# Performance work log

Hardware: AMD Instinct MI355X
Metric: run time of the kernel (lower is better)

Reference implementation:

```python
import jax, jax.numpy as jnp
import numpy as np

EOS_IDX = 2
B, LAYERS, HEADS, SEQ = 1, 33, 20, 512


def setup_inputs() -> dict:
    key = jax.random.key(0)
    k1, k2, k3, k4 = jax.random.split(key, 4)
    tokens = jax.random.randint(k1, (B, SEQ), 0, 30)
    attentions = jax.random.normal(k2, (B, LAYERS, HEADS, SEQ, SEQ), dtype=jnp.float32)
    weight = jax.random.normal(k3, (LAYERS * HEADS,), dtype=jnp.float32) * 0.05
    bias = jax.random.normal(k4, (1,), dtype=jnp.float32) * 0.05
    return {"tokens": tokens, "attentions": attentions, "weight": weight, "bias": bias}


def reference(tokens, attentions, weight, bias):
    b, nl, nh, s, _ = attentions.shape
    # mask out positions at/after EOS token pairs
    eos = (tokens != EOS_IDX).astype(attentions.dtype)           # [B, S]
    mask2d = eos[:, None, :] * eos[:, :, None]                   # [B, S, S]
    att = attentions * mask2d[:, None, None, :, :]
    # [..., :-1, :-1] then [..., 1:, 1:] == drop first and last positions
    att = att[..., 1:-1, 1:-1]                                   # [B, L, H, S-2, S-2]
    att = att.reshape(b, nl * nh, s - 2, s - 2)                  # [B, F, s2, s2]
    # symmetrize
    sym = att + jnp.swapaxes(att, -1, -2)
    # average product correction
    a1 = sym.sum(-1, keepdims=True)                              # [B, F, s2, 1]
    a2 = sym.sum(-2, keepdims=True)                              # [B, F, 1, s2]
    a12 = sym.sum((-1, -2), keepdims=True)                       # [B, F, 1, 1]
    norm = sym - a1 * a2 / a12
    logits = jnp.einsum('bfij,f->bij', norm, weight) + bias[0]
    return jax.nn.sigmoid(logits)                                # [B, s2, s2]
```

## Files before the change

kernel.cpp:

```cpp
#include <hip/hip_runtime.h>
#include <math.h>

#define SEQ   512
#define NF    660
#define CROP  510
#define EOSI  2
#define RT    16
#define GH    20
#define NT_   32
#define NG    33

typedef float f4 __attribute__((ext_vector_type(4)));
typedef float f2 __attribute__((ext_vector_type(2)));

#define BARRIER_LGKM() asm volatile("s_waitcnt lgkmcnt(0)\n\ts_barrier" ::: "memory")

#define LOADP(buf, f, prow) do {                                              \
    const float* _b = A + ((size_t)(f) << 18) + ((size_t)(prow) << 9);        \
    buf[0] = *(const f4*)(_b + 4 * lane);                                     \
    buf[1] = *(const f4*)(_b + 256 + 4 * lane);                               \
    buf[2] = *(const f4*)(_b + 512 + 4 * lane);                               \
    buf[3] = *(const f4*)(_b + 768 + 4 * lane);                               \
} while (0)

#define COMP(buf, wf, cacc, wa, POFF, h) do {                                 \
    _Pragma("unroll")                                                         \
    for (int rr = 0; rr < 2; ++rr) {                                          \
        const float mi = mrow[(POFF) * 2 + rr];                               \
        f4 x0 = buf[2 * rr], x1 = buf[2 * rr + 1];                            \
        float vals[8] = {x0[0], x0[1], x0[2], x0[3],                          \
                         x1[0], x1[1], x1[2], x1[3]};                         \
        float rs = 0.f;                                                       \
        _Pragma("unroll")                                                     \
        for (int e = 0; e < 8; ++e) {                                         \
            const float v = vals[e];                                          \
            wa[rr][e] += (wf) * v;                                            \
            rs += mskv[e] * v;                                                \
            cacc[e] += mi * v;                                                \
        }                                                                     \
        _Pragma("unroll")                                                     \
        for (int off = 32; off > 0; off >>= 1)                                \
            rs += __shfl_down(rs, off, 64);                                   \
        if (lane == 0)                                                        \
            rowstage[h][wave * 4 + (POFF) * 2 + rr] = rs;                     \
    }                                                                         \
} while (0)

__global__ __launch_bounds__(256) void pass1_kernel(
    const float* __restrict__ A, const int* __restrict__ tokens,
    const float* __restrict__ weight,
    float* __restrict__ WApart, float* __restrict__ rowsum, float* __restrict__ colpart)
{
    __shared__ float msk[SEQ];
    __shared__ float col_lds[2][4][SEQ];
    __shared__ float colstage[GH][SEQ];
    __shared__ float rowstage[GH][RT];

    const int t = blockIdx.x, g = blockIdx.y;
    const int tid = threadIdx.x, wave = tid >> 6, lane = tid & 63;

    for (int j = tid; j < SEQ; j += 256)
        msk[j] = (j >= 1 && j <= SEQ - 2 && tokens[j] != EOSI) ? 1.f : 0.f;
    BARRIER_LGKM();

    float mskv[8];
    #pragma unroll
    for (int e = 0; e < 8; ++e)
        mskv[e] = msk[(e >> 2) * 256 + 4 * lane + (e & 3)];

    const int row0 = t * RT + wave * 4;
    const float mrow[4] = {msk[row0], msk[row0 + 1], msk[row0 + 2], msk[row0 + 3]};

    float waLo[2][8], waHi[2][8];
    #pragma unroll
    for (int r = 0; r < 2; ++r)
        #pragma unroll
        for (int e = 0; e < 8; ++e) { waLo[r][e] = 0.f; waHi[r][e] = 0.f; }

    f4 bufA[4], bufB[4];
    const int fbase = g * GH;
    LOADP(bufA, fbase, row0);

    for (int h = 0; h < GH; ++h) {
        const int f = fbase + h;
        const float wf = weight[f];
        float cacc[8] = {0, 0, 0, 0, 0, 0, 0, 0};

        LOADP(bufB, f, row0 + 2);
        COMP(bufA, wf, cacc, waLo, 0, h);
        if (h < GH - 1) LOADP(bufA, f + 1, row0);
        COMP(bufB, wf, cacc, waHi, 1, h);

        const int pp = h & 1;
        #pragma unroll
        for (int e = 0; e < 8; ++e)
            col_lds[pp][wave][(e >> 2) * 256 + 4 * lane + (e & 3)] = cacc[e];
        BARRIER_LGKM();
        {
            const int c = 2 * tid;
            f2 s;
            s[0] = col_lds[pp][0][c]     + col_lds[pp][1][c]
                 + col_lds[pp][2][c]     + col_lds[pp][3][c];
            s[1] = col_lds[pp][0][c + 1] + col_lds[pp][1][c + 1]
                 + col_lds[pp][2][c + 1] + col_lds[pp][3][c + 1];
            *(f2*)&colstage[h][c] = s;
        }
    }

    BARRIER_LGKM();

    {
        float* __restrict__ dst = colpart + ((size_t)t * NF + fbase) * SEQ;
        const float* __restrict__ srcl = &colstage[0][0];
        #pragma unroll
        for (int it = 0; it < 10; ++it) {
            const int fl = (it * 256 + tid) * 4;
            *(f4*)(dst + fl) = *(const f4*)(srcl + fl);
        }
    }
    #pragma unroll
    for (int it = 0; it < 2; ++it) {
        const int e = it * 256 + tid;
        if (e < GH * RT) {
            const int h = e >> 4, r = e & 15;
            rowsum[((size_t)(fbase + h) << 9) + t * RT + r] = rowstage[h][r];
        }
    }
    float* __restrict__ wp = WApart + (size_t)g * SEQ * SEQ;
    #pragma unroll
    for (int rr = 0; rr < 2; ++rr) {
        f4 l0 = {waLo[rr][0], waLo[rr][1], waLo[rr][2], waLo[rr][3]};
        f4 l1 = {waLo[rr][4], waLo[rr][5], waLo[rr][6], waLo[rr][7]};
        *(f4*)(wp + ((size_t)(row0 + rr) << 9) + 4 * lane) = l0;
        *(f4*)(wp + ((size_t)(row0 + rr) << 9) + 256 + 4 * lane) = l1;
        f4 h0 = {waHi[rr][0], waHi[rr][1], waHi[rr][2], waHi[rr][3]};
        f4 h1 = {waHi[rr][4], waHi[rr][5], waHi[rr][6], waHi[rr][7]};
        *(f4*)(wp + ((size_t)(row0 + 2 + rr) << 9) + 4 * lane) = h0;
        *(f4*)(wp + ((size_t)(row0 + 2 + rr) << 9) + 256 + 4 * lane) = h1;
    }
}

__global__ __launch_bounds__(512) void kernel2(
    const float* __restrict__ WApart, float* __restrict__ WA,
    const float* __restrict__ rowsum, const float* __restrict__ colpart,
    const int* __restrict__ tokens, const float* __restrict__ weight,
    float* __restrict__ a1, float* __restrict__ sfac)
{
    __shared__ float part[8];
    const int b = blockIdx.x, tid = threadIdx.x;
    if (b < 128) {
        const size_t idx4 = (size_t)b * 512 + tid;
        f4 a = *(const f4*)(WApart + 4 * idx4);
        #pragma unroll 8
        for (int g = 1; g < NG; ++g) {
            f4 x = *(const f4*)(WApart + (size_t)g * (SEQ * SEQ) + 4 * idx4);
            a += x;
        }
        *(f4*)(WA + 4 * idx4) = a;
    } else {
        const int f = b - 128, j = tid;
        float cs = 0.f;
        #pragma unroll 8
        for (int t = 0; t < NT_; ++t)
            cs += colpart[((size_t)t * NF + f) * SEQ + j];
        const float m = (j >= 1 && j <= SEQ - 2 && tokens[j] != EOSI) ? 1.f : 0.f;
        const float v = m * (rowsum[((size_t)f << 9) + j] + cs);
        a1[((size_t)f << 9) + j] = v;
        float s = v;
        #pragma unroll
        for (int off = 32; off > 0; off >>= 1)
            s += __shfl_down(s, off, 64);
        const int wave = tid >> 6, lane = tid & 63;
        if (lane == 0) part[wave] = s;
        __syncthreads();
        if (tid == 0) {
            float a12 = 0.f;
            #pragma unroll
            for (int k = 0; k < 8; ++k) a12 += part[k];
            sfac[f] = weight[f] / a12;
        }
    }
}

__global__ __launch_bounds__(256) void pass3_kernel(
    const float* __restrict__ WA, const float* __restrict__ a1,
    const float* __restrict__ sfac, const int* __restrict__ tokens,
    const float* __restrict__ bias, float* __restrict__ out)
{
    const int TI = blockIdx.y * 16;
    const int TJ = blockIdx.x * 16;
    const int tid = threadIdx.x;
    const int tx = tid & 15, ty = tid >> 4;

    __shared__ float u_s[32][17];
    __shared__ float v_s[32][17];

    float acc = 0.f;

    for (int f0 = 0; f0 < NF; f0 += 32) {
        #pragma unroll
        for (int c = 0; c < 4; ++c) {
            const int e = c * 256 + tid;
            const int arr = e >> 9, ff = (e >> 4) & 31, ii = e & 15;
            const int f = f0 + ff;
            float val = 0.f;
            if (f < NF) {
                if (arr == 0) {
                    int Iu = TI + 1 + ii; if (Iu > SEQ - 1) Iu = SEQ - 1;
                    val = a1[((size_t)f << 9) + Iu] * sfac[f];
                } else {
                    int Ju = TJ + 1 + ii; if (Ju > SEQ - 1) Ju = SEQ - 1;
                    val = a1[((size_t)f << 9) + Ju];
                }
            }
            if (arr == 0) u_s[ff][ii] = val; else v_s[ff][ii] = val;
        }
        __syncthreads();
        #pragma unroll
        for (int ff = 0; ff < 32; ++ff)
            acc += u_s[ff][ty] * v_s[ff][tx];
        __syncthreads();
    }

    const int i = TI + ty, j = TJ + tx;
    if (i < CROP && j < CROP) {
        const int I = i + 1, J = j + 1;
        const float mi = (tokens[I] != EOSI) ? 1.f : 0.f;
        const float mj = (tokens[J] != EOSI) ? 1.f : 0.f;
        const float first = mi * mj * (WA[((size_t)I << 9) + J] + WA[((size_t)J << 9) + I]);
        const float logit = first - acc + bias[0];
        out[(size_t)i * CROP + j] = 1.f / (1.f + expf(-logit));
    }
}

extern "C" void kernel_launch(void* const* d_in, const int* in_sizes, int n_in,
                              void* d_out, int out_size, void* d_ws, size_t ws_size,
                              hipStream_t stream) {
    const int*   tokens = (const int*)d_in[0];
    const float* A      = (const float*)d_in[1];
    const float* weight = (const float*)d_in[2];
    const float* bias   = (const float*)d_in[3];
    float* out = (float*)d_out;

    float* WApart  = (float*)d_ws;
    float* colpart = WApart + (size_t)NG * SEQ * SEQ;
    float* WA      = colpart + (size_t)NT_ * NF * SEQ;
    float* rowsum  = WA + (size_t)SEQ * SEQ;
    float* a1      = rowsum + (size_t)NF * SEQ;
    float* sfac    = a1 + (size_t)NF * SEQ;

    dim3 g1(NT_, NG);
    pass1_kernel<<<g1, 256, 0, stream>>>(A, tokens, weight, WApart, rowsum, colpart);

    kernel2<<<128 + NF, 512, 0, stream>>>(WApart, WA, rowsum, colpart, tokens, weight, a1, sfac);

    dim3 g3(32, 32);
    pass3_kernel<<<g3, 256, 0, stream>>>(WA, a1, sfac, tokens, bias, out);
}
```

Measured before the change: 215.7 us.

## Prefetch a whole next head slab and stream column partials incrementally

The pass-1 loop now loads all four rows of the next head into a second register buffer while the current head is computed, instead of splitting each head into two half-row loads. Column-sum staging shrinks from 20 heads to a double-buffered 4-head ring that is written to global memory during the loop rather than all at the end. Launch bounds request 3 blocks per CU. The aim is deeper memory-latency hiding, less LDS per block and higher occupancy. The cost is more registers for the 8-vector buffers, which may spill under the occupancy hint.

```diff
diff --git a/kernel.cpp b/kernel.cpp
--- a/kernel.cpp
+++ b/kernel.cpp
@@ -15,18 +15,22 @@
 
 #define BARRIER_LGKM() asm volatile("s_waitcnt lgkmcnt(0)\n\ts_barrier" ::: "memory")
 
-#define LOADP(buf, f, prow) do {                                              \
-    const float* _b = A + ((size_t)(f) << 18) + ((size_t)(prow) << 9);        \
+#define LOADP8(buf, f) do {                                                   \
+    const float* _b = A + ((size_t)(f) << 18) + ((size_t)row0 << 9);          \
     buf[0] = *(const f4*)(_b + 4 * lane);                                     \
     buf[1] = *(const f4*)(_b + 256 + 4 * lane);                               \
     buf[2] = *(const f4*)(_b + 512 + 4 * lane);                               \
     buf[3] = *(const f4*)(_b + 768 + 4 * lane);                               \
-} while (0)
-
-#define COMP(buf, wf, cacc, wa, POFF, h) do {                                 \
+    buf[4] = *(const f4*)(_b + 1024 + 4 * lane);                              \
+    buf[5] = *(const f4*)(_b + 1280 + 4 * lane);                              \
+    buf[6] = *(const f4*)(_b + 1536 + 4 * lane);                              \
+    buf[7] = *(const f4*)(_b + 1792 + 4 * lane);                              \
+} while (0)
+
+#define COMP8(buf, wf, cacc, h) do {                                          \
     _Pragma("unroll")                                                         \
-    for (int rr = 0; rr < 2; ++rr) {                                          \
-        const float mi = mrow[(POFF) * 2 + rr];                               \
+    for (int rr = 0; rr < 4; ++rr) {                                          \
+        const float mi = mrow[rr];                                            \
         f4 x0 = buf[2 * rr], x1 = buf[2 * rr + 1];                            \
         float vals[8] = {x0[0], x0[1], x0[2], x0[3],                          \
                          x1[0], x1[1], x1[2], x1[3]};                         \
@@ -34,30 +38,55 @@
         _Pragma("unroll")                                                     \
         for (int e = 0; e < 8; ++e) {                                         \
             const float v = vals[e];                                          \
-            wa[rr][e] += (wf) * v;                                            \
+            wa_acc[rr][e] += (wf) * v;                                        \
             rs += mskv[e] * v;                                                \
             cacc[e] += mi * v;                                                \
         }                                                                     \
         _Pragma("unroll")                                                     \
         for (int off = 32; off > 0; off >>= 1)                                \
             rs += __shfl_down(rs, off, 64);                                   \
-        if (lane == 0)                                                        \
-            rowstage[h][wave * 4 + (POFF) * 2 + rr] = rs;                     \
+        if (lane == 0) rowstage[h][wave * 4 + rr] = rs;                       \
     }                                                                         \
 } while (0)
 
-__global__ __launch_bounds__(256) void pass1_kernel(
+#define FLUSHCOL(q) do {                                                      \
+    float* __restrict__ _dst = colpart + ((size_t)t * NF + fbase + 4 * (q)) * SEQ; \
+    const float* __restrict__ _src = &colstage[(q) & 1][0][0];                \
+    *(f4*)(_dst + 4 * tid)        = *(const f4*)(_src + 4 * tid);             \
+    *(f4*)(_dst + 1024 + 4 * tid) = *(const f4*)(_src + 1024 + 4 * tid);      \
+} while (0)
+
+#define COMBINE(cacc, h) do {                                                 \
+    const int pp = (h) & 1;                                                   \
+    _Pragma("unroll")                                                         \
+    for (int e = 0; e < 8; ++e)                                               \
+        col_lds[pp][wave][(e >> 2) * 256 + 4 * lane + (e & 3)] = cacc[e];     \
+    BARRIER_LGKM();                                                           \
+    if (((h) & 3) == 0 && (h) > 0) FLUSHCOL((h) / 4 - 1);                     \
+    {                                                                         \
+        const int c = 2 * tid;                                                \
+        f2 s;                                                                 \
+        s[0] = col_lds[pp][0][c]     + col_lds[pp][1][c]                      \
+             + col_lds[pp][2][c]     + col_lds[pp][3][c];                     \
+        s[1] = col_lds[pp][0][c + 1] + col_lds[pp][1][c + 1]                  \
+             + col_lds[pp][2][c + 1] + col_lds[pp][3][c + 1];                 \
+        *(f2*)&colstage[((h) >> 2) & 1][(h) & 3][c] = s;                      \
+    }                                                                         \
+} while (0)
+
+__global__ __launch_bounds__(256, 3) void pass1_kernel(
     const float* __restrict__ A, const int* __restrict__ tokens,
     const float* __restrict__ weight,
     float* __restrict__ WApart, float* __restrict__ rowsum, float* __restrict__ colpart)
 {
     __shared__ float msk[SEQ];
     __shared__ float col_lds[2][4][SEQ];
-    __shared__ float colstage[GH][SEQ];
+    __shared__ float colstage[2][4][SEQ];
     __shared__ float rowstage[GH][RT];
 
     const int t = blockIdx.x, g = blockIdx.y;
     const int tid = threadIdx.x, wave = tid >> 6, lane = tid & 63;
+    const int fbase = g * GH;
 
     for (int j = tid; j < SEQ; j += 256)
         msk[j] = (j >= 1 && j <= SEQ - 2 && tokens[j] != EOSI) ? 1.f : 0.f;
@@ -71,53 +100,34 @@
     const int row0 = t * RT + wave * 4;
     const float mrow[4] = {msk[row0], msk[row0 + 1], msk[row0 + 2], msk[row0 + 3]};
 
-    float waLo[2][8], waHi[2][8];
-    #pragma unroll
-    for (int r = 0; r < 2; ++r)
-        #pragma unroll
-        for (int e = 0; e < 8; ++e) { waLo[r][e] = 0.f; waHi[r][e] = 0.f; }
-
-    f4 bufA[4], bufB[4];
-    const int fbase = g * GH;
-    LOADP(bufA, fbase, row0);
-
-    for (int h = 0; h < GH; ++h) {
-        const int f = fbase + h;
-        const float wf = weight[f];
-        float cacc[8] = {0, 0, 0, 0, 0, 0, 0, 0};
-
-        LOADP(bufB, f, row0 + 2);
-        COMP(bufA, wf, cacc, waLo, 0, h);
-        if (h < GH - 1) LOADP(bufA, f + 1, row0);
-        COMP(bufB, wf, cacc, waHi, 1, h);
-
-        const int pp = h & 1;
-        #pragma unroll
-        for (int e = 0; e < 8; ++e)
-            col_lds[pp][wave][(e >> 2) * 256 + 4 * lane + (e & 3)] = cacc[e];
-        BARRIER_LGKM();
-        {
-            const int c = 2 * tid;
-            f2 s;
-            s[0] = col_lds[pp][0][c]     + col_lds[pp][1][c]
-                 + col_lds[pp][2][c]     + col_lds[pp][3][c];
-            s[1] = col_lds[pp][0][c + 1] + col_lds[pp][1][c + 1]
-                 + col_lds[pp][2][c + 1] + col_lds[pp][3][c + 1];
-            *(f2*)&colstage[h][c] = s;
-        }
+    float wa_acc[4][8];
+    #pragma unroll
+    for (int r = 0; r < 4; ++r)
+        #pragma unroll
+        for (int e = 0; e < 8; ++e) wa_acc[r][e] = 0.f;
+
+    f4 bufA[8], bufB[8];
+    LOADP8(bufA, fbase);
+
+    #pragma unroll 1
+    for (int hh = 0; hh < 10; ++hh) {
+        const int h0 = 2 * hh, h1 = h0 + 1;
+
+        float cacc0[8] = {0, 0, 0, 0, 0, 0, 0, 0};
+        LOADP8(bufB, fbase + h1);
+        COMP8(bufA, weight[fbase + h0], cacc0, h0);
+        COMBINE(cacc0, h0);
+
+        float cacc1[8] = {0, 0, 0, 0, 0, 0, 0, 0};
+        if (hh < 9) LOADP8(bufA, fbase + h0 + 2);
+        COMP8(bufB, weight[fbase + h1], cacc1, h1);
+        COMBINE(cacc1, h1);
     }
 
     BARRIER_LGKM();
 
-    {
-        float* __restrict__ dst = colpart + ((size_t)t * NF + fbase) * SEQ;
-        const float* __restrict__ srcl = &colstage[0][0];
-        #pragma unroll
-        for (int it = 0; it < 10; ++it) {
-            const int fl = (it * 256 + tid) * 4;
-            *(f4*)(dst + fl) = *(const f4*)(srcl + fl);
-        }
-    }
+    FLUSHCOL(4);
+
     #pragma unroll
     for (int it = 0; it < 2; ++it) {
         const int e = it * 256 + tid;
@@ -128,15 +138,11 @@
     }
     float* __restrict__ wp = WApart + (size_t)g * SEQ * SEQ;
     #pragma unroll
-    for (int rr = 0; rr < 2; ++rr) {
-        f4 l0 = {waLo[rr][0], waLo[rr][1], waLo[rr][2], waLo[rr][3]};
-        f4 l1 = {waLo[rr][4], waLo[rr][5], waLo[rr][6], waLo[rr][7]};
-        *(f4*)(wp + ((size_t)(row0 + rr) << 9) + 4 * lane) = l0;
-        *(f4*)(wp + ((size_t)(row0 + rr) << 9) + 256 + 4 * lane) = l1;
-        f4 h0 = {waHi[rr][0], waHi[rr][1], waHi[rr][2], waHi[rr][3]};
-        f4 h1 = {waHi[rr][4], waHi[rr][5], waHi[rr][6], waHi[rr][7]};
-        *(f4*)(wp + ((size_t)(row0 + 2 + rr) << 9) + 4 * lane) = h0;
-        *(f4*)(wp + ((size_t)(row0 + 2 + rr) << 9) + 256 + 4 * lane) = h1;
+    for (int rr = 0; rr < 4; ++rr) {
+        f4 o0 = {wa_acc[rr][0], wa_acc[rr][1], wa_acc[rr][2], wa_acc[rr][3]};
+        f4 o1 = {wa_acc[rr][4], wa_acc[rr][5], wa_acc[rr][6], wa_acc[rr][7]};
+        *(f4*)(wp + ((size_t)(row0 + rr) << 9) + 4 * lane) = o0;
+        *(f4*)(wp + ((size_t)(row0 + rr) << 9) + 256 + 4 * lane) = o1;
     }
 }
 
```

After: 227.0 us. +5.2%, slower.
